# Performance work log

Hardware: AMD Instinct MI355X
Metric: run time of the kernel (lower is better)

The kernel has to match this reference:

```python
import jax, jax.numpy as jnp
import numpy as np

MEMORY_SIZE = 2000
SHAPE = (512, 8, 8)
D = int(np.prod(SHAPE))  # 32768
LAM = 0.0005  # hard-shrink threshold (1/memory_size convention)
EPS = 1e-12   # F.normalize eps


def _l2_normalize(x, axis):
    # matches F.normalize(p=2): x / max(||x||, eps)
    n = jnp.sqrt(jnp.sum(x * x, axis=axis, keepdims=True))
    return x / jnp.maximum(n, EPS)


def _hard_shrink(x):
    return jnp.where(jnp.abs(x) > LAM, x, jnp.zeros_like(x))


def setup_inputs() -> dict:
    key = jax.random.key(0)
    k1, k2 = jax.random.split(key)
    feature = jax.random.normal(k1, (256, *SHAPE), dtype=jnp.float32)
    memory = jax.random.normal(k2, (MEMORY_SIZE, D), dtype=jnp.float32)
    return {"feature": feature, "memory": memory}


def reference(feature, memory):
    B = feature.shape[0]
    flat = feature.reshape(B, -1)                     # [B, D]
    fn = _l2_normalize(flat, axis=1)                  # [B, D]
    mn = _l2_normalize(memory, axis=1)                # [M, D]
    w = jnp.einsum('bd,md->bm', fn, mn)               # cosine similarity [B, M]
    w = jax.nn.softmax(w, axis=1)
    w = _hard_shrink(w)
    w = jax.nn.softmax(w, axis=1)
    mem_feat = jnp.einsum('bm,md->bd', w, memory)     # [B, D]
    mem_feat = mem_feat.reshape(B, *SHAPE)
    return (mem_feat, w)
```

## Files before the change

kernel.cpp:

```cpp
#include <hip/hip_runtime.h>
#include <math.h>


#define D_DIM 32768
#define B_DIM 256
#define M_DIM 2000
#define M_PAD 2048
#define NS1 16
#define KSLAB (D_DIM / NS1)
#define LAM 0.0005f
#define LDB 72

typedef __attribute__((ext_vector_type(8))) short bf16x8;
typedef __attribute__((ext_vector_type(4))) float f32x4;

#define GLOBAL_AS __attribute__((address_space(1)))
#define LDS_AS __attribute__((address_space(3)))

__device__ __forceinline__ void cp_async16(const void* g, void* l) {
  __builtin_amdgcn_global_load_lds((const GLOBAL_AS unsigned int*)g,
                                   (LDS_AS unsigned int*)l, 16, 0, 0);
}

__device__ __forceinline__ unsigned short f2bf(float f) {
  union { float f; unsigned u; } v; v.f = f;
  unsigned r = v.u + 0x7FFFu + ((v.u >> 16) & 1u);
  return (unsigned short)(r >> 16);
}

__global__ __launch_bounds__(256) void zero_kernel(float* __restrict__ p, int n) {
  int i = blockIdx.x * 256 + threadIdx.x;
  if (i < n) p[i] = 0.f;
}

__global__ __launch_bounds__(256) void prep_feat_kernel(const float* __restrict__ src,
                                                        unsigned short* __restrict__ dst,
                                                        float* __restrict__ rn_inv) {
  const size_t row = blockIdx.x;
  const int t = threadIdx.x;
  const float4* p = (const float4*)(src + row * (size_t)D_DIM);
  ushort4* q = (ushort4*)(dst + row * (size_t)D_DIM);
  float s = 0.f;
  for (int i = t; i < D_DIM / 4; i += 256) {
    float4 v = p[i];
    s = fmaf(v.x, v.x, s); s = fmaf(v.y, v.y, s);
    s = fmaf(v.z, v.z, s); s = fmaf(v.w, v.w, s);
    ushort4 b; b.x = f2bf(v.x); b.y = f2bf(v.y); b.z = f2bf(v.z); b.w = f2bf(v.w);
    q[i] = b;
  }
  #pragma unroll
  for (int off = 32; off > 0; off >>= 1) s += __shfl_down(s, off, 64);
  __shared__ float partial[4];
  if ((t & 63) == 0) partial[t >> 6] = s;
  __syncthreads();
  if (t == 0) {
    float tt = partial[0] + partial[1] + partial[2] + partial[3];
    rn_inv[row] = 1.0f / fmaxf(sqrtf(tt), 1e-12f);
  }
}

__global__ __launch_bounds__(256, 3) void gemm1_fused(const unsigned short* __restrict__ F16,
                                                      const float* __restrict__ mem,
                                                      float* __restrict__ Spart,
                                                      float* __restrict__ rnm_sq) {
  __shared__ __align__(16) unsigned short Asm[256 * 64];
  __shared__ __align__(16) unsigned short Bsm[64 * LDB];
  const int t = threadIdx.x;
  const int m0 = blockIdx.x * 64;
  const int kbase = blockIdx.y * KSLAB;
  const int wid = t >> 6, lane = t & 63;
  const int lr = lane & 15, kq = lane >> 4;
  const int l8 = lane & 7, lrow = lane >> 3;

  const int brow = t >> 2;
  const int bcol = (t & 3) * 16;
  const int gm = m0 + brow;
  const bool bvalid = gm < M_DIM;
  const float* Bg = mem + (size_t)gm * D_DIM + kbase + bcol;

  const unsigned short* Ab = F16 + (size_t)(64 * wid + lrow) * D_DIM + kbase + (l8 ^ lrow) * 8;

  f32x4 acc[4][4] = {};
  float ss = 0.f;

  for (int kt = 0; kt < KSLAB / 64; kt++) {
    const int kk = kt * 64;
    __syncthreads();
    #pragma unroll
    for (int i = 0; i < 8; i++)
      cp_async16(Ab + kk + (size_t)(8 * i) * D_DIM, &Asm[(64 * wid + 8 * i) * 64]);

    float4 v[4];
    #pragma unroll
    for (int j = 0; j < 4; j++)
      v[j] = bvalid ? *(const float4*)(Bg + kk + 4 * j) : make_float4(0.f, 0.f, 0.f, 0.f);
    #pragma unroll
    for (int j = 0; j < 4; j++) {
      ss = fmaf(v[j].x, v[j].x, ss); ss = fmaf(v[j].y, v[j].y, ss);
      ss = fmaf(v[j].z, v[j].z, ss); ss = fmaf(v[j].w, v[j].w, ss);
      ushort4 c; c.x = f2bf(v[j].x); c.y = f2bf(v[j].y);
      c.z = f2bf(v[j].z); c.w = f2bf(v[j].w);
      *(ushort4*)&Bsm[brow * LDB + bcol + 4 * j] = c;
    }
    __syncthreads();

    bf16x8 bfr[2][4];
    #pragma unroll
    for (int h = 0; h < 2; h++)
      #pragma unroll
      for (int ni = 0; ni < 4; ni++)
        bfr[h][ni] = *(const bf16x8*)&Bsm[(ni * 16 + lr) * LDB + h * 32 + kq * 8];
    #pragma unroll
    for (int mi = 0; mi < 4; mi++) {
      #pragma unroll
      for (int h = 0; h < 2; h++) {
        const int sw = ((h * 4 + kq) ^ (lr & 7)) * 8;
        const bf16x8 af = *(const bf16x8*)&Asm[(wid * 64 + mi * 16 + lr) * 64 + sw];
        #pragma unroll
        for (int ni = 0; ni < 4; ni++)
          acc[mi][ni] = __builtin_amdgcn_mfma_f32_16x16x32_bf16(af, bfr[h][ni], acc[mi][ni], 0, 0, 0);
      }
    }
  }

  ss += __shfl_down(ss, 2, 4);
  ss += __shfl_down(ss, 1, 4);
  if ((t & 3) == 0 && bvalid) atomicAdd(&rnm_sq[gm], ss);

  float* Sp = Spart + (size_t)blockIdx.y * (B_DIM * M_PAD);
  #pragma unroll
  for (int mi = 0; mi < 4; mi++) {
    const int b0 = wid * 64 + mi * 16 + kq * 4;
    #pragma unroll
    for (int ni = 0; ni < 4; ni++) {
      const int col = m0 + ni * 16 + lr;
      #pragma unroll
      for (int j = 0; j < 4; j++)
        Sp[(size_t)(b0 + j) * M_PAD + col] = acc[mi][ni][j];
    }
  }
}

__device__ __forceinline__ float block_reduce(float x, bool is_max, float* red,
                                              int wid, int lane) {
  #pragma unroll
  for (int off = 32; off > 0; off >>= 1) {
    float o = __shfl_down(x, off, 64);
    x = is_max ? fmaxf(x, o) : (x + o);
  }
  __syncthreads();
  if (lane == 0) red[wid] = x;
  __syncthreads();
  return is_max ? fmaxf(fmaxf(red[0], red[1]), fmaxf(red[2], red[3]))
                : (red[0] + red[1] + red[2] + red[3]);
}

__global__ __launch_bounds__(256) void softmax_kernel(const float* __restrict__ Spart,
                                                      const float* __restrict__ rnf,
                                                      const float* __restrict__ rnm_sq,
                                                      float* __restrict__ wout,
                                                      unsigned short* __restrict__ wbf) {
  const int b = blockIdx.x;
  const int t = threadIdx.x;
  const int wid = t >> 6, lane = t & 63;
  const float sf = rnf[b];
  __shared__ float red[4];

  float v[8];
  #pragma unroll
  for (int g = 0; g < 2; g++) {
    const int mq = g * 1024 + 4 * t;
    f32x4 a = {0.f, 0.f, 0.f, 0.f};
    #pragma unroll
    for (int s = 0; s < NS1; s++)
      a += *(const f32x4*)&Spart[(size_t)s * (B_DIM * M_PAD) + (size_t)b * M_PAD + mq];
    #pragma unroll
    for (int j = 0; j < 4; j++) {
      const int m = mq + j;
      const float msc = 1.0f / fmaxf(sqrtf(rnm_sq[m]), 1e-12f);
      v[g * 4 + j] = (m < M_DIM) ? a[j] * (sf * msc) : -INFINITY;
    }
  }
  float mx = v[0];
  #pragma unroll
  for (int i = 1; i < 8; i++) mx = fmaxf(mx, v[i]);
  mx = block_reduce(mx, true, red, wid, lane);

  float e[8]; float sum = 0.f;
  #pragma unroll
  for (int i = 0; i < 8; i++) { e[i] = expf(v[i] - mx); sum += e[i]; }
  sum = block_reduce(sum, false, red, wid, lane);
  const float inv = 1.f / sum;

  float s2[8];
  #pragma unroll
  for (int i = 0; i < 8; i++) {
    float w1 = e[i] * inv;
    s2[i] = (w1 > LAM) ? w1 : 0.f;
  }
  float mx2 = 0.f;
  #pragma unroll
  for (int i = 0; i < 8; i++) mx2 = fmaxf(mx2, s2[i]);
  mx2 = block_reduce(mx2, true, red, wid, lane);

  float e2[8]; float sum2 = 0.f;
  #pragma unroll
  for (int g = 0; g < 2; g++)
    #pragma unroll
    for (int j = 0; j < 4; j++) {
      const int i = g * 4 + j;
      const int m = g * 1024 + 4 * t + j;
      e2[i] = (m < M_DIM) ? expf(s2[i] - mx2) : 0.f;
      sum2 += e2[i];
    }
  sum2 = block_reduce(sum2, false, red, wid, lane);
  const float inv2 = 1.f / sum2;

  #pragma unroll
  for (int g = 0; g < 2; g++) {
    const int mq = g * 1024 + 4 * t;
    float4 wq; ushort4 bq;
    float* wp = (float*)&wq;
    #pragma unroll
    for (int j = 0; j < 4; j++) {
      const float w2 = e2[g * 4 + j] * inv2;
      wp[j] = w2;
      ((unsigned short*)&bq)[j] = f2bf(w2);
    }
    if (mq + 3 < M_DIM) *(float4*)&wout[(size_t)b * M_DIM + mq] = wq;
    *(ushort4*)&wbf[(size_t)b * M_PAD + mq] = bq;
  }
}

__global__ __launch_bounds__(256, 3) void gemm2_kernel(const unsigned short* __restrict__ W,
                                                       const float* __restrict__ mem,
                                                       float* __restrict__ C) {
  __shared__ __align__(16) unsigned short Wsm[256 * 64];
  __shared__ __align__(16) unsigned short Bt[64 * 64];
  const int t = threadIdx.x;
  const int n0 = blockIdx.x * 64;
  const int wid = t >> 6, lane = t & 63;
  const int lr = lane & 15, kq = lane >> 4;
  const int l8 = lane & 7, lrow = lane >> 3;

  const unsigned short* Wb = W + (size_t)(64 * wid + lrow) * M_PAD + (l8 ^ lrow) * 8;

  const int bn = t & 63;
  const int kc = t >> 6;
  const float* Bg = mem + (size_t)(kc * 16) * D_DIM + n0 + bn;

  f32x4 acc[4][4] = {};

  for (int k0 = 0; k0 < M_PAD; k0 += 64) {
    __syncthreads();
    #pragma unroll
    for (int i = 0; i < 8; i++)
      cp_async16(Wb + k0 + (size_t)(8 * i) * M_PAD, &Wsm[(64 * wid + 8 * i) * 64]);

    bf16x8 kb0, kb1;
    #pragma unroll
    for (int j = 0; j < 8; j++) {
      const int k = k0 + kc * 16 + j;
      const float f = (k < M_DIM) ? Bg[(size_t)(k0 + j) * D_DIM] : 0.f;
      kb0[j] = (short)f2bf(f);
    }
    #pragma unroll
    for (int j = 8; j < 16; j++) {
      const int k = k0 + kc * 16 + j;
      const float f = (k < M_DIM) ? Bg[(size_t)(k0 + j) * D_DIM] : 0.f;
      kb1[j - 8] = (short)f2bf(f);
    }
    *(bf16x8*)&Bt[bn * 64 + (((kc * 2 + 0) ^ (bn & 7)) * 8)] = kb0;
    *(bf16x8*)&Bt[bn * 64 + (((kc * 2 + 1) ^ (bn & 7)) * 8)] = kb1;
    __syncthreads();

    bf16x8 bfr[2][4];
    #pragma unroll
    for (int h = 0; h < 2; h++)
      #pragma unroll
      for (int ni = 0; ni < 4; ni++)
        bfr[h][ni] = *(const bf16x8*)&Bt[(ni * 16 + lr) * 64 + (((h * 4 + kq) ^ (lr & 7)) * 8)];
    #pragma unroll
    for (int mi = 0; mi < 4; mi++) {
      #pragma unroll
      for (int h = 0; h < 2; h++) {
        const int sw = ((h * 4 + kq) ^ (lr & 7)) * 8;
        const bf16x8 af = *(const bf16x8*)&Wsm[(wid * 64 + mi * 16 + lr) * 64 + sw];
        #pragma unroll
        for (int ni = 0; ni < 4; ni++)
          acc[mi][ni] = __builtin_amdgcn_mfma_f32_16x16x32_bf16(af, bfr[h][ni], acc[mi][ni], 0, 0, 0);
      }
    }
  }
  #pragma unroll
  for (int mi = 0; mi < 4; mi++) {
    const int b0 = wid * 64 + mi * 16 + kq * 4;
    #pragma unroll
    for (int ni = 0; ni < 4; ni++) {
      const int col = n0 + ni * 16 + lr;
      #pragma unroll
      for (int j = 0; j < 4; j++)
        C[(size_t)(b0 + j) * D_DIM + col] = acc[mi][ni][j];
    }
  }
}

extern "C" void kernel_launch(void* const* d_in, const int* in_sizes, int n_in,
                              void* d_out, int out_size, void* d_ws, size_t ws_size,
                              hipStream_t stream) {
  const float* feature = (const float*)d_in[0];
  const float* memory  = (const float*)d_in[1];
  float* out_feat = (float*)d_out;
  float* out_w = out_feat + (size_t)B_DIM * D_DIM;

  char* ws = (char*)d_ws;
  unsigned short* F16 = (unsigned short*)ws;
  float* Spart        = (float*)(ws + 16777216ull);
  unsigned short* Wbf = (unsigned short*)(ws + 50331648ull);
  float* rnm_sq       = (float*)(ws + 51380224ull);
  float* rnf          = (float*)(ws + 51388416ull);

  zero_kernel<<<(M_PAD + 255) / 256, 256, 0, stream>>>(rnm_sq, M_PAD);
  prep_feat_kernel<<<B_DIM, 256, 0, stream>>>(feature, F16, rnf);
  gemm1_fused<<<dim3(M_PAD / 64, NS1), 256, 0, stream>>>(F16, memory, Spart, rnm_sq);
  softmax_kernel<<<B_DIM, 256, 0, stream>>>(Spart, rnf, rnm_sq, out_w, Wbf);
  gemm2_kernel<<<D_DIM / 64, 256, 0, stream>>>(Wbf, memory, out_feat);
}
```

Before: 491.2 us.

## Store split-K partials as bf16, remap gemm1 blocks per XCD, fold zeroing into prep

The split-K partial sums from gemm1 are now written as bf16 rather than fp32, halving the partial-buffer traffic that softmax must read back. gemm1 moves to a 1D grid whose block index is remapped so each XCD handles two K-slabs, aiming at better L2 reuse of the feature slab. The separate zeroing launch is merged into prep_feat, and the bounds checks on loads are replaced by clamped addresses. Rounding partials to bf16 before the reduction lowers the precision of the cosine scores that feed the softmax.

```diff
diff --git a/kernel.cpp b/kernel.cpp
--- a/kernel.cpp
+++ b/kernel.cpp
@@ -28,16 +28,18 @@
   return (unsigned short)(r >> 16);
 }
 
-__global__ __launch_bounds__(256) void zero_kernel(float* __restrict__ p, int n) {
-  int i = blockIdx.x * 256 + threadIdx.x;
-  if (i < n) p[i] = 0.f;
+__device__ __forceinline__ float bf2f(unsigned short h) {
+  union { unsigned u; float f; } v; v.u = ((unsigned)h) << 16;
+  return v.f;
 }
 
 __global__ __launch_bounds__(256) void prep_feat_kernel(const float* __restrict__ src,
                                                         unsigned short* __restrict__ dst,
-                                                        float* __restrict__ rn_inv) {
+                                                        float* __restrict__ rn_inv,
+                                                        float* __restrict__ rnm_sq) {
   const size_t row = blockIdx.x;
   const int t = threadIdx.x;
+  if (t < 8) rnm_sq[(blockIdx.x << 3) + t] = 0.f;
   const float4* p = (const float4*)(src + row * (size_t)D_DIM);
   ushort4* q = (ushort4*)(dst + row * (size_t)D_DIM);
   float s = 0.f;
@@ -61,13 +63,16 @@
 
 __global__ __launch_bounds__(256, 3) void gemm1_fused(const unsigned short* __restrict__ F16,
                                                       const float* __restrict__ mem,
-                                                      float* __restrict__ Spart,
+                                                      unsigned short* __restrict__ Spart,
                                                       float* __restrict__ rnm_sq) {
   __shared__ __align__(16) unsigned short Asm[256 * 64];
   __shared__ __align__(16) unsigned short Bsm[64 * LDB];
   const int t = threadIdx.x;
-  const int m0 = blockIdx.x * 64;
-  const int kbase = blockIdx.y * KSLAB;
+  const int bid = blockIdx.x;
+  const int xcd = bid & 7, slot = bid >> 3;
+  const int ysplit = xcd * 2 + (slot >> 5);
+  const int m0 = (slot & 31) * 64;
+  const int kbase = ysplit * KSLAB;
   const int wid = t >> 6, lane = t & 63;
   const int lr = lane & 15, kq = lane >> 4;
   const int l8 = lane & 7, lrow = lane >> 3;
@@ -76,14 +81,15 @@
   const int bcol = (t & 3) * 16;
   const int gm = m0 + brow;
   const bool bvalid = gm < M_DIM;
-  const float* Bg = mem + (size_t)gm * D_DIM + kbase + bcol;
+  const float* Bg = mem + (size_t)(bvalid ? gm : 0) * D_DIM + kbase + bcol;
 
   const unsigned short* Ab = F16 + (size_t)(64 * wid + lrow) * D_DIM + kbase + (l8 ^ lrow) * 8;
 
   f32x4 acc[4][4] = {};
   float ss = 0.f;
 
-  for (int kt = 0; kt < KSLAB / 64; kt++) {
+  const int NT = KSLAB / 64;
+  for (int kt = 0; kt < NT; kt++) {
     const int kk = kt * 64;
     __syncthreads();
     #pragma unroll
@@ -92,8 +98,7 @@
 
     float4 v[4];
     #pragma unroll
-    for (int j = 0; j < 4; j++)
-      v[j] = bvalid ? *(const float4*)(Bg + kk + 4 * j) : make_float4(0.f, 0.f, 0.f, 0.f);
+    for (int j = 0; j < 4; j++) v[j] = *(const float4*)(Bg + kk + 4 * j);
     #pragma unroll
     for (int j = 0; j < 4; j++) {
       ss = fmaf(v[j].x, v[j].x, ss); ss = fmaf(v[j].y, v[j].y, ss);
@@ -127,7 +132,7 @@
   ss += __shfl_down(ss, 1, 4);
   if ((t & 3) == 0 && bvalid) atomicAdd(&rnm_sq[gm], ss);
 
-  float* Sp = Spart + (size_t)blockIdx.y * (B_DIM * M_PAD);
+  unsigned short* Sp = Spart + (size_t)ysplit * (B_DIM * M_PAD);
   #pragma unroll
   for (int mi = 0; mi < 4; mi++) {
     const int b0 = wid * 64 + mi * 16 + kq * 4;
@@ -136,7 +141,7 @@
       const int col = m0 + ni * 16 + lr;
       #pragma unroll
       for (int j = 0; j < 4; j++)
-        Sp[(size_t)(b0 + j) * M_PAD + col] = acc[mi][ni][j];
+        Sp[(size_t)(b0 + j) * M_PAD + col] = f2bf(acc[mi][ni][j]);
     }
   }
 }
@@ -155,7 +160,7 @@
                 : (red[0] + red[1] + red[2] + red[3]);
 }
 
-__global__ __launch_bounds__(256) void softmax_kernel(const float* __restrict__ Spart,
+__global__ __launch_bounds__(256) void softmax_kernel(const unsigned short* __restrict__ Spart,
                                                       const float* __restrict__ rnf,
                                                       const float* __restrict__ rnm_sq,
                                                       float* __restrict__ wout,
@@ -170,15 +175,18 @@
   #pragma unroll
   for (int g = 0; g < 2; g++) {
     const int mq = g * 1024 + 4 * t;
-    f32x4 a = {0.f, 0.f, 0.f, 0.f};
-    #pragma unroll
-    for (int s = 0; s < NS1; s++)
-      a += *(const f32x4*)&Spart[(size_t)s * (B_DIM * M_PAD) + (size_t)b * M_PAD + mq];
+    float a0 = 0.f, a1 = 0.f, a2 = 0.f, a3 = 0.f;
+    #pragma unroll
+    for (int s = 0; s < NS1; s++) {
+      const ushort4 u = *(const ushort4*)&Spart[(size_t)s * (B_DIM * M_PAD) + (size_t)b * M_PAD + mq];
+      a0 += bf2f(u.x); a1 += bf2f(u.y); a2 += bf2f(u.z); a3 += bf2f(u.w);
+    }
+    const float aa[4] = {a0, a1, a2, a3};
     #pragma unroll
     for (int j = 0; j < 4; j++) {
       const int m = mq + j;
       const float msc = 1.0f / fmaxf(sqrtf(rnm_sq[m]), 1e-12f);
-      v[g * 4 + j] = (m < M_DIM) ? a[j] * (sf * msc) : -INFINITY;
+      v[g * 4 + j] = (m < M_DIM) ? aa[j] * (sf * msc) : -INFINITY;
     }
   }
   float mx = v[0];
@@ -247,11 +255,13 @@
 
   const int bn = t & 63;
   const int kc = t >> 6;
-  const float* Bg = mem + (size_t)(kc * 16) * D_DIM + n0 + bn;
+  const float* Bg2 = mem + n0 + bn;
 
   f32x4 acc[4][4] = {};
 
-  for (int k0 = 0; k0 < M_PAD; k0 += 64) {
+  const int NT = M_PAD / 64;
+  for (int it = 0; it < NT; it++) {
+    const int k0 = it * 64;
     __syncthreads();
     #pragma unroll
     for (int i = 0; i < 8; i++)
@@ -261,14 +271,14 @@
     #pragma unroll
     for (int j = 0; j < 8; j++) {
       const int k = k0 + kc * 16 + j;
-      const float f = (k < M_DIM) ? Bg[(size_t)(k0 + j) * D_DIM] : 0.f;
-      kb0[j] = (short)f2bf(f);
+      const int r = (k < M_DIM) ? k : 0;
+      kb0[j] = (short)f2bf(Bg2[(size_t)r * D_DIM]);
     }
     #pragma unroll
     for (int j = 8; j < 16; j++) {
       const int k = k0 + kc * 16 + j;
-      const float f = (k < M_DIM) ? Bg[(size_t)(k0 + j) * D_DIM] : 0.f;
-      kb1[j - 8] = (short)f2bf(f);
+      const int r = (k < M_DIM) ? k : 0;
+      kb1[j - 8] = (short)f2bf(Bg2[(size_t)r * D_DIM]);
     }
     *(bf16x8*)&Bt[bn * 64 + (((kc * 2 + 0) ^ (bn & 7)) * 8)] = kb0;
     *(bf16x8*)&Bt[bn * 64 + (((kc * 2 + 1) ^ (bn & 7)) * 8)] = kb1;
@@ -315,14 +325,13 @@
 
   char* ws = (char*)d_ws;
   unsigned short* F16 = (unsigned short*)ws;
-  float* Spart        = (float*)(ws + 16777216ull);
+  unsigned short* Spart = (unsigned short*)(ws + 16777216ull);
   unsigned short* Wbf = (unsigned short*)(ws + 50331648ull);
   float* rnm_sq       = (float*)(ws + 51380224ull);
   float* rnf          = (float*)(ws + 51388416ull);
 
-  zero_kernel<<<(M_PAD + 255) / 256, 256, 0, stream>>>(rnm_sq, M_PAD);
-  prep_feat_kernel<<<B_DIM, 256, 0, stream>>>(feature, F16, rnf);
-  gemm1_fused<<<dim3(M_PAD / 64, NS1), 256, 0, stream>>>(F16, memory, Spart, rnm_sq);
+  prep_feat_kernel<<<B_DIM, 256, 0, stream>>>(feature, F16, rnf, rnm_sq);
+  gemm1_fused<<<512, 256, 0, stream>>>(F16, memory, Spart, rnm_sq);
   softmax_kernel<<<B_DIM, 256, 0, stream>>>(Spart, rnf, rnm_sq, out_w, Wbf);
   gemm2_kernel<<<D_DIM / 64, 256, 0, stream>>>(Wbf, memory, out_feat);
 }
```

Measured after the change: 495.0 us. About the same (+0.8%).
